# Performance work log

Measured on AMD Instinct MI355X. Metric: run time of the kernel, lower is better.

## Reference

```python
import jax, jax.numpy as jnp
import numpy as np

B, C, H, W = 8, 64, 224, 224
M, N = 7, 7          # kernel_size
S = 2                # stride
NEG_INF = -1e30      # aggregation identity for max-plus (finite, fp-safe); unused since pad=0


def setup_inputs() -> dict:
    key = jax.random.key(0)
    kx, kw = jax.random.split(key)
    x = jax.random.normal(kx, (B, C, H, W), dtype=jnp.float32)
    w = jax.random.normal(kw, (1, C, M, N), dtype=jnp.float32)  # (B_w=1, C_out, M, N)
    return {"x": x, "w": w}


def reference(x, w):
    """SemiPool2d with max-plus semifield, padding='valid', ceil_mode=False.

    out[b,c,p,q] = max_{i<M, j<N} ( x[b,c, p*S+i, q*S+j] + w[0,c,i,j] )
    """
    Bf, Cin, Hx, Wx = x.shape
    _, Cout, Mk, Nk = w.shape
    H_out = (Hx - Mk) // S + 1
    W_out = (Wx - Nk) // S + 1
    # pad_h = max((H_out-1)*S + M - H, 0) = 0 for these dims -> no padding needed.
    # Unfold: gather the MN strided shifts (small fixed loop over kernel taps).
    patches = jnp.stack(
        [x[:, :, i:i + S * (H_out - 1) + 1:S, j:j + S * (W_out - 1) + 1:S]
         for i in range(Mk) for j in range(Nk)],
        axis=2,
    )  # (B, C, M*N, H_out, W_out)
    # weighting = '+', aggregation = max over the window taps (dim 3 in original)
    weighted = patches + w.reshape(1, Cout, Mk * Nk, 1, 1)
    return jnp.max(weighted, axis=2)  # (B, C_out, H_out, W_out)
```

## Files before the change

kernel.cpp:

```cpp
#include <hip/hip_runtime.h>


#define HH 224
#define WW 224
#define HO 109
#define WO 109
#define CC 64
#define PBAND 16
#define NB 7
#define INROWS 37
#define BANDF (INROWS*WW)
#define WCH 518

__global__ __launch_bounds__(256) void semipool_kernel(
    const float* __restrict__ x,
    const float* __restrict__ w,
    float* __restrict__ out)
{
    __shared__ float smem[2][BANDF];

    const int tid  = threadIdx.x;
    const int wv   = tid >> 6;
    const int lane = tid & 63;
    const int pairIdx = blockIdx.x >> 9;
    const int bc      = blockIdx.x & 511;
    const int bandB   = pairIdx + 4;
    const bool hasB   = (bandB < NB);

    const int p0A = pairIdx * PBAND;
    int p0B = bandB * PBAND; if (p0B > HO - PBAND) p0B = HO - PBAND;

    const float* __restrict__ xc = x + bc * (HH * WW);

    {
        const float* src = xc + (2 * p0A) * WW;
#pragma unroll
        for (int it = 0; it < 9; ++it) {
            int off = it * 64 + lane;
            if (off < WCH) {
                int c = wv * WCH + off;
                __builtin_amdgcn_global_load_lds(
                    (const __attribute__((address_space(1))) void*)(src + 4 * c),
                    (__attribute__((address_space(3))) void*)(&smem[0][4 * c]),
                    16, 0, 0);
            }
        }
    }
    if (hasB) {
        const float* src = xc + (2 * p0B) * WW;
#pragma unroll
        for (int it = 0; it < 9; ++it) {
            int off = it * 64 + lane;
            if (off < WCH) {
                int c = wv * WCH + off;
                __builtin_amdgcn_global_load_lds(
                    (const __attribute__((address_space(1))) void*)(src + 4 * c),
                    (__attribute__((address_space(3))) void*)(&smem[1][4 * c]),
                    16, 0, 0);
            }
        }
    }

    const float* __restrict__ wp = w + (bc & (CC - 1)) * 49;
    float wr[49];
#pragma unroll
    for (int k = 0; k < 49; ++k) wr[k] = wp[k];

    if (hasB) asm volatile("s_waitcnt vmcnt(9)" ::: "memory");
    else      asm volatile("s_waitcnt vmcnt(0)" ::: "memory");
    __builtin_amdgcn_sched_barrier(0);
    __builtin_amdgcn_s_barrier();
    __builtin_amdgcn_sched_barrier(0);

    int q = tid & 127; if (q > WO - 1) q = WO - 1;
    const int ph   = tid >> 7;
    const int colb = 2 * q;

    float accA[8], accB[8];

#define COMPUTE_BAND(BUF, ACC)                                            \
    do {                                                                  \
        _Pragma("unroll")                                                 \
        for (int a = 0; a < 8; ++a) ACC[a] = -1e30f;                      \
        _Pragma("unroll")                                                 \
        for (int r = 0; r < 21; ++r) {                                    \
            const float* lr = &smem[BUF][(16 * ph + r) * WW + colb];      \
            float xr[8];                                                  \
            _Pragma("unroll")                                             \
            for (int k = 0; k < 4; ++k) {                                 \
                float2 v = *reinterpret_cast<const float2*>(lr + 2 * k);  \
                xr[2 * k] = v.x; xr[2 * k + 1] = v.y;                     \
            }                                                             \
            _Pragma("unroll")                                             \
            for (int pp = 0; pp < 8; ++pp) {                              \
                int i = r - 2 * pp;                                       \
                if (i >= 0 && i < 7) {                                    \
                    float s0 = xr[0] + wr[i * 7 + 0];                     \
                    float s1 = xr[1] + wr[i * 7 + 1];                     \
                    float s2 = xr[2] + wr[i * 7 + 2];                     \
                    float s3 = xr[3] + wr[i * 7 + 3];                     \
                    float s4 = xr[4] + wr[i * 7 + 4];                     \
                    float s5 = xr[5] + wr[i * 7 + 5];                     \
                    float s6 = xr[6] + wr[i * 7 + 6];                     \
                    float t0 = fmaxf(fmaxf(s0, s1), s2);                  \
                    float t1 = fmaxf(fmaxf(s3, s4), s5);                  \
                    float t2 = fmaxf(fmaxf(t0, t1), s6);                  \
                    ACC[pp] = fmaxf(ACC[pp], t2);                         \
                }                                                         \
            }                                                             \
        }                                                                 \
    } while (0)

#define STORE_BAND(P0B, ACC)                                              \
    do {                                                                  \
        float* orow = out + (bc * HO + (P0B) + 8 * ph) * WO + q;          \
        _Pragma("unroll")                                                 \
        for (int pp = 0; pp < 8; ++pp) orow[pp * WO] = ACC[pp];           \
    } while (0)

    COMPUTE_BAND(0, accA);

    if (hasB) {
        asm volatile("s_waitcnt vmcnt(0)" ::: "memory");
        __builtin_amdgcn_sched_barrier(0);
        __builtin_amdgcn_s_barrier();
        __builtin_amdgcn_sched_barrier(0);
        STORE_BAND(p0A, accA);
        COMPUTE_BAND(1, accB);
        STORE_BAND(p0B, accB);
    } else {
        STORE_BAND(p0A, accA);
    }
}

extern "C" void kernel_launch(void* const* d_in, const int* in_sizes, int n_in,
                              void* d_out, int out_size, void* d_ws, size_t ws_size,
                              hipStream_t stream) {
    const float* x = (const float*)d_in[0];
    const float* w = (const float*)d_in[1];
    float* out = (float*)d_out;

    int blocks = 4 * 512;
    semipool_kernel<<<blocks, 256, 0, stream>>>(x, w, out);
}
```

Measured before the change: 31.21 us.

## Use one band per block with split-half LDS load overlapped with compute

```diff
diff --git a/kernel.cpp b/kernel.cpp
--- a/kernel.cpp
+++ b/kernel.cpp
@@ -9,55 +9,52 @@
 #define PBAND 16
 #define NB 7
 #define INROWS 37
-#define BANDF (INROWS*WW)
-#define WCH 518
+#define LDSF (INROWS*WW)
+#define H1_PER_WAVE 294
+#define H1_INSTR 5
+#define H1_CHUNKS 1176
+#define H2_PER_WAVE 224
+#define H2_INSTR 4
 
 __global__ __launch_bounds__(256) void semipool_kernel(
     const float* __restrict__ x,
     const float* __restrict__ w,
     float* __restrict__ out)
 {
-    __shared__ float smem[2][BANDF];
+    __shared__ float smem[LDSF];
 
     const int tid  = threadIdx.x;
     const int wv   = tid >> 6;
     const int lane = tid & 63;
-    const int pairIdx = blockIdx.x >> 9;
-    const int bc      = blockIdx.x & 511;
-    const int bandB   = pairIdx + 4;
-    const bool hasB   = (bandB < NB);
+    const int band = blockIdx.x >> 9;
+    const int bc   = blockIdx.x & 511;
 
-    const int p0A = pairIdx * PBAND;
-    int p0B = bandB * PBAND; if (p0B > HO - PBAND) p0B = HO - PBAND;
+    int p0b = band * PBAND;
+    if (p0b > HO - PBAND) p0b = HO - PBAND;
+    const int row0 = 2 * p0b;
 
-    const float* __restrict__ xc = x + bc * (HH * WW);
+    const float* src = x + (bc * HH + row0) * WW;
 
-    {
-        const float* src = xc + (2 * p0A) * WW;
 #pragma unroll
-        for (int it = 0; it < 9; ++it) {
-            int off = it * 64 + lane;
-            if (off < WCH) {
-                int c = wv * WCH + off;
-                __builtin_amdgcn_global_load_lds(
-                    (const __attribute__((address_space(1))) void*)(src + 4 * c),
-                    (__attribute__((address_space(3))) void*)(&smem[0][4 * c]),
-                    16, 0, 0);
-            }
+    for (int it = 0; it < H1_INSTR; ++it) {
+        int off = it * 64 + lane;
+        if (off < H1_PER_WAVE) {
+            int c = wv * H1_PER_WAVE + off;
+            __builtin_amdgcn_global_load_lds(
+                (const __attribute__((address_space(1))) void*)(src + 4 * c),
+                (__attribute__((address_space(3))) void*)(smem + 4 * c),
+                16, 0, 0);
         }
     }
-    if (hasB) {
-        const float* src = xc + (2 * p0B) * WW;
 #pragma unroll
-        for (int it = 0; it < 9; ++it) {
-            int off = it * 64 + lane;
-            if (off < WCH) {
-                int c = wv * WCH + off;
-                __builtin_amdgcn_global_load_lds(
-                    (const __attribute__((address_space(1))) void*)(src + 4 * c),
-                    (__attribute__((address_space(3))) void*)(&smem[1][4 * c]),
-                    16, 0, 0);
-            }
+    for (int it = 0; it < H2_INSTR; ++it) {
+        int off = it * 64 + lane;
+        if (off < H2_PER_WAVE) {
+            int c = H1_CHUNKS + wv * H2_PER_WAVE + off;
+            __builtin_amdgcn_global_load_lds(
+                (const __attribute__((address_space(1))) void*)(src + 4 * c),
+                (__attribute__((address_space(3))) void*)(smem + 4 * c),
+                16, 0, 0);
         }
     }
 
@@ -66,8 +63,7 @@
 #pragma unroll
     for (int k = 0; k < 49; ++k) wr[k] = wp[k];
 
-    if (hasB) asm volatile("s_waitcnt vmcnt(9)" ::: "memory");
-    else      asm volatile("s_waitcnt vmcnt(0)" ::: "memory");
+    asm volatile("s_waitcnt vmcnt(4)" ::: "memory");
     __builtin_amdgcn_sched_barrier(0);
     __builtin_amdgcn_s_barrier();
     __builtin_amdgcn_sched_barrier(0);
@@ -76,15 +72,15 @@
     const int ph   = tid >> 7;
     const int colb = 2 * q;
 
-    float accA[8], accB[8];
+    float acc[8];
+#pragma unroll
+    for (int a = 0; a < 8; ++a) acc[a] = -1e30f;
 
-#define COMPUTE_BAND(BUF, ACC)                                            \
+#define COMPUTE(BASE)                                                     \
     do {                                                                  \
         _Pragma("unroll")                                                 \
-        for (int a = 0; a < 8; ++a) ACC[a] = -1e30f;                      \
-        _Pragma("unroll")                                                 \
         for (int r = 0; r < 21; ++r) {                                    \
-            const float* lr = &smem[BUF][(16 * ph + r) * WW + colb];      \
+            const float* lr = smem + ((BASE) + r) * WW + colb;            \
             float xr[8];                                                  \
             _Pragma("unroll")                                             \
             for (int k = 0; k < 4; ++k) {                                 \
@@ -105,32 +101,25 @@
                     float t0 = fmaxf(fmaxf(s0, s1), s2);                  \
                     float t1 = fmaxf(fmaxf(s3, s4), s5);                  \
                     float t2 = fmaxf(fmaxf(t0, t1), s6);                  \
-                    ACC[pp] = fmaxf(ACC[pp], t2);                         \
+                    acc[pp] = fmaxf(acc[pp], t2);                         \
                 }                                                         \
             }                                                             \
         }                                                                 \
     } while (0)
 
-#define STORE_BAND(P0B, ACC)                                              \
-    do {                                                                  \
-        float* orow = out + (bc * HO + (P0B) + 8 * ph) * WO + q;          \
-        _Pragma("unroll")                                                 \
-        for (int pp = 0; pp < 8; ++pp) orow[pp * WO] = ACC[pp];           \
-    } while (0)
+    if (ph == 0) COMPUTE(0);
 
-    COMPUTE_BAND(0, accA);
+    asm volatile("s_waitcnt vmcnt(0)" ::: "memory");
+    __builtin_amdgcn_sched_barrier(0);
+    __builtin_amdgcn_s_barrier();
+    __builtin_amdgcn_sched_barrier(0);
 
-    if (hasB) {
-        asm volatile("s_waitcnt vmcnt(0)" ::: "memory");
-        __builtin_amdgcn_sched_barrier(0);
-        __builtin_amdgcn_s_barrier();
-        __builtin_amdgcn_sched_barrier(0);
-        STORE_BAND(p0A, accA);
-        COMPUTE_BAND(1, accB);
-        STORE_BAND(p0B, accB);
-    } else {
-        STORE_BAND(p0A, accA);
-    }
+    if (ph == 1) COMPUTE(16);
+
+    float* __restrict__ orow = out + (bc * HO + p0b + 8 * ph) * WO + q;
+#pragma unroll
+    for (int pp = 0; pp < 8; ++pp)
+        orow[pp * WO] = acc[pp];
 }
 
 extern "C" void kernel_launch(void* const* d_in, const int* in_sizes, int n_in,
@@ -140,6 +129,5 @@
     const float* w = (const float*)d_in[1];
     float* out = (float*)d_out;
 
-    int blocks = 4 * 512;
-    semipool_kernel<<<blocks, 256, 0, stream>>>(x, w, out);
+    semipool_kernel<<<NB * 512, 256, 0, stream>>>(x, w, out);
 }
```

Measured after the change: 32.02 us. +2.6%, slower.
